# Kernel optimization log

Measured on AMD Instinct MI355X. Metric: run time of the kernel, lower is better.

Reference implementation:

```python
import jax, jax.numpy as jnp
import numpy as np

N_WIRES = 16
VAR_DEPTH = 2
BATCH = 16


def _param_sizes():
    sizes = []
    n = N_WIRES
    lay = 0
    while n > 1:
        sizes.append(4 * int(np.ceil(N_WIRES / 2 ** lay)) * VAR_DEPTH)
        n = (n + 1) // 2
        lay += 1
    return sizes  # [128, 64, 32, 16]


def _apply_1q(psi, gate, w):
    # psi: (B, 2, ..., 2); gate: (2,2) complex; wire w lives on axis w+1
    psi = jnp.moveaxis(psi, w + 1, -1)
    psi = jnp.einsum('...j,ij->...i', psi, gate)
    return jnp.moveaxis(psi, -1, w + 1)


def _rx(psi, th, w):
    c = jnp.cos(th / 2).astype(jnp.complex64)
    s = jnp.sin(th / 2).astype(jnp.complex64)
    gate = jnp.stack([jnp.stack([c, -1j * s]), jnp.stack([-1j * s, c])])
    return _apply_1q(psi, gate, w)


def _rz(psi, th, w):
    ph = jnp.exp(0.5j * th * jnp.array([-1.0, 1.0], jnp.float32)).astype(jnp.complex64)
    shape = [1] * psi.ndim
    shape[w + 1] = 2
    return psi * ph.reshape(shape)


def _rzz(psi, th, wa, wb):
    # diag(e^{-i t/2}, e^{i t/2}, e^{i t/2}, e^{-i t/2}) -> sign = -1 if bits equal else +1
    sgn = jnp.array([[-1.0, 1.0], [1.0, -1.0]], jnp.float32)
    ph = jnp.exp(0.5j * th * sgn).astype(jnp.complex64)  # symmetric, transpose-safe
    a, b = min(wa, wb) + 1, max(wa, wb) + 1
    shape = [1] * psi.ndim
    shape[a] = 2
    shape[b] = 2
    return psi * ph.reshape(shape)


def _cnot(psi, c, t):
    p0 = jax.lax.slice_in_dim(psi, 0, 1, axis=c + 1)
    p1 = jax.lax.slice_in_dim(psi, 1, 2, axis=c + 1)
    return jnp.concatenate([p0, jnp.flip(p1, axis=t + 1)], axis=c + 1)


def _conv_layer(psi, params, active):
    n = len(active)
    for d in range(VAR_DEPTH):
        for j in range(n):
            base = 4 * j + d * 4 * n
            psi = _rx(psi, params[base + 0], active[j])
            psi = _rz(psi, params[base + 1], active[j])
            psi = _rx(psi, params[base + 2], active[j])
        for bg in (0, 1):
            for j in range(bg, n, 2):
                jn = (j + 1) % n  # ring coupling (wraps last->first)
                base = 4 * j + d * 4 * n
                psi = _rzz(psi, params[base + 3], active[j], active[jn])
    return psi


def _pool(psi, active):
    for j in range(0, len(active), 2):
        if j + 1 < len(active):
            psi = _cnot(psi, active[j], active[j + 1])
    return psi, active[::2]


def _forward(psi, params_list):
    active = list(range(N_WIRES))
    for p in params_list:
        psi = _conv_layer(psi, p, active)
        if len(active) > 1:
            psi, active = _pool(psi, active)
    w = active[0]  # measure Z on the surviving wire (wire 0)
    prob = psi.real ** 2 + psi.imag ** 2
    axes = tuple(a for a in range(1, psi.ndim) if a != w + 1)
    p2 = prob.sum(axis=axes)  # (B, 2)
    return p2[:, 0] - p2[:, 1]


def setup_inputs() -> dict:
    key = jax.random.key(0)
    ks = jax.random.split(key, 8)
    dim = 2 ** N_WIRES
    x_re = jax.random.normal(ks[0], (BATCH, dim), dtype=jnp.float32)
    x_im = jax.random.normal(ks[1], (BATCH, dim), dtype=jnp.float32)
    nrm = jnp.sqrt(jnp.sum(x_re ** 2 + x_im ** 2, axis=1, keepdims=True))
    x_re = x_re / nrm
    x_im = x_im / nrm
    sizes = _param_sizes()
    two_pi = 2.0 * np.pi
    params = [jax.random.uniform(ks[2 + i], (sizes[i],), dtype=jnp.float32) * two_pi
              for i in range(len(sizes))]
    return {"x_re": x_re, "x_im": x_im,
            "params0": params[0], "params1": params[1],
            "params2": params[2], "params3": params[3]}


def reference(x_re, x_im, params0, params1, params2, params3):
    psi = (x_re + 1j * x_im).astype(jnp.complex64)
    psi = psi.reshape((BATCH,) + (2,) * N_WIRES)
    return _forward(psi, [params0, params1, params2, params3])
```

## Files before the change

kernel.cpp:

```cpp
#include <hip/hip_runtime.h>


#define DEV __device__ __forceinline__

__device__ static const unsigned char G_CP[60] = {
  15,14,13,12,11,10,9,8,7,6,5,4,3,2,1,0,
  15,14,13,12,11,10,9,8,7,6,5,4,3,2,1,0,
  15,13,11,9,7,5,3,1,
  15,13,11,9,7,5,3,1,
  15,11,7,3,
  15,11,7,3,
  15,7,
  15,7
};
__device__ static const unsigned char G_CQ[60] = {
  14,13,12,11,10,9,8,7,6,5,4,3,2,1,0,15,
  14,13,12,11,10,9,8,7,6,5,4,3,2,1,0,15,
  13,11,9,7,5,3,1,15,
  13,11,9,7,5,3,1,15,
  11,7,3,15,
  11,7,3,15,
  7,15,
  7,15
};

DEV float2 F2(float x, float y){ float2 r; r.x = x; r.y = y; return r; }
DEV float2 cmulf(float2 a, float2 b){ return F2(a.x*b.x - a.y*b.y, a.x*b.y + a.y*b.x); }
DEV int swz(int j){ return j ^ ((j>>4)&15) ^ ((j>>8)&15); }
DEV int sw2(int m){
  return m ^ ((m>>9)&1) ^ (((m>>11)&1)<<1)
           ^ ((((m>>3)&1)^((m>>8)&1))<<2)
           ^ ((((m>>4)&1)^((m>>5)&1)^((m>>10)&1))<<3);
}

#if __has_builtin(__builtin_amdgcn_permlane32_swap)
#define HAVE_PLS 1
DEV void plswap01(float &x0, float &x1){
  auto r = __builtin_amdgcn_permlane32_swap(__float_as_uint(x0), __float_as_uint(x1), false, false);
  x0 = __uint_as_float((unsigned)r[0]);
  x1 = __uint_as_float((unsigned)r[1]);
}
#else
#define HAVE_PLS 0
#endif

template<int SB>
DEV void gate4(float2* a, const float* __restrict__ g){
  float u00r=g[0],u00i=g[1],u01r=g[2],u01i=g[3],u10r=g[4],u10i=g[5],u11r=g[6],u11i=g[7];
  #pragma unroll
  for (int m=0;m<2;m++){
    int i0 = (SB==0) ? (m<<1) : m;
    int i1 = i0 | (1<<SB);
    float2 x0=a[i0], x1=a[i1];
    a[i0] = F2(u00r*x0.x - u00i*x0.y + u01r*x1.x - u01i*x1.y,
               u00r*x0.y + u00i*x0.x + u01r*x1.y + u01i*x1.x);
    a[i1] = F2(u10r*x0.x - u10i*x0.y + u11r*x1.x - u11i*x1.y,
               u10r*x0.y + u10i*x0.x + u11r*x1.y + u11i*x1.x);
  }
}

DEV void lgate(float2* a, const float* __restrict__ g, int mask, int lane){
  bool h = (lane & mask) != 0;
  float Ar = h ? g[6] : g[0], Ai = h ? g[7] : g[1];
  float Br = h ? g[4] : g[2], Bi = h ? g[5] : g[3];
  #pragma unroll
  for (int s=0;s<4;s++){
    float px = __shfl_xor(a[s].x, mask);
    float py = __shfl_xor(a[s].y, mask);
    a[s] = F2(Ar*a[s].x - Ai*a[s].y + Br*px - Bi*py,
              Ar*a[s].y + Ai*a[s].x + Br*py + Bi*px);
  }
}

DEV void lgate32(float2* a, const float* __restrict__ g, int lane){
#if HAVE_PLS
  bool h = (lane & 32) != 0;
  float c0r = h ? g[4] : g[0], c0i = h ? g[5] : g[1];
  float c1r = h ? g[6] : g[2], c1i = h ? g[7] : g[3];
  #pragma unroll
  for (int s=0;s<4;s++){
    float x0x = a[s].x, x1x = a[s].x, x0y = a[s].y, x1y = a[s].y;
    plswap01(x0x, x1x); plswap01(x0y, x1y);
    a[s] = F2(c0r*x0x - c0i*x0y + c1r*x1x - c1i*x1y,
              c0r*x0y + c0i*x0x + c1r*x1y + c1i*x1x);
  }
#else
  lgate(a, g, 32, lane);
#endif
}

DEV void cswap(float2* a, int cmask, int tmask, int lane){
  bool c = (lane & cmask) != 0;
  #pragma unroll
  for (int s=0;s<4;s++){
    float px = __shfl_xor(a[s].x, tmask);
    float py = __shfl_xor(a[s].y, tmask);
    if (c){ a[s].x = px; a[s].y = py; }
  }
}

template<int C0,int N0,int C1,int N1,unsigned M0,unsigned M1>
DEV void diagx(float2* a, const float* __restrict__ hh, unsigned Ib){
  const unsigned rm = M0|M1;
  float base = 0.f;
  #pragma unroll
  for (int k=C0;k<C0+N0;k++){
    const int p=G_CP[k], q=G_CQ[k];
    if (!(((1u<<p)|(1u<<q)) & rm)){
      float h = hh[k];
      base += (((Ib>>p)^(Ib>>q))&1u) ? h : -h;
    }
  }
  #pragma unroll
  for (int k=C1;k<C1+N1;k++){
    const int p=G_CP[k], q=G_CQ[k];
    if (!(((1u<<p)|(1u<<q)) & rm)){
      float h = hh[k];
      base += (((Ib>>p)^(Ib>>q))&1u) ? h : -h;
    }
  }
  #pragma unroll
  for (int r=0;r<4;r++){
    unsigned Ir = Ib ^ ((r&1)?M0:0u) ^ ((r&2)?M1:0u);
    float ph = base;
    #pragma unroll
    for (int k=C0;k<C0+N0;k++){
      const int p=G_CP[k], q=G_CQ[k];
      if (((1u<<p)|(1u<<q)) & rm){
        float h = hh[k];
        ph += (((Ir>>p)^(Ir>>q))&1u) ? h : -h;
      }
    }
    #pragma unroll
    for (int k=C1;k<C1+N1;k++){
      const int p=G_CP[k], q=G_CQ[k];
      if (((1u<<p)|(1u<<q)) & rm){
        float h = hh[k];
        ph += (((Ir>>p)^(Ir>>q))&1u) ? h : -h;
      }
    }
    float c, s;
    __sincosf(ph, &s, &c);
    a[r] = cmulf(a[r], F2(c, s));
  }
}

DEV void build_entry(float* sh, const float* __restrict__ p0, const float* __restrict__ p1,
                     const float* __restrict__ p2, const float* __restrict__ p3, int g){
  int d, j, n; const float* P;
  if (g < 32)      { n=16; d=(g>>4)&1; j=g&15; P=p0; }
  else if (g < 48) { n=8;  d=(g>>3)&1; j=g&7;  P=p1; }
  else if (g < 56) { n=4;  d=(g>>2)&1; j=g&3;  P=p2; }
  else             { n=2;  d=(g>>1)&1; j=g&1;  P=p3; }
  int base = 4*j + 4*n*d;
  float th0 = P[base+0], th1 = P[base+1], th2 = P[base+2], th3 = P[base+3];
  float c0,s0,ca,sa,c2,s2;
  sincosf(0.5f*th0, &s0, &c0);
  sincosf(0.5f*th1, &sa, &ca);
  sincosf(0.5f*th2, &s2, &c2);
  float B00r =  ca*c0, B00i = -sa*c0;
  float B01r = -sa*s0, B01i = -ca*s0;
  float B10r =  sa*s0, B10i = -ca*s0;
  float B11r =  ca*c0, B11i =  sa*c0;
  float* o8 = sh + g*8;
  o8[0]=c2*B00r + s2*B10i; o8[1]=c2*B00i - s2*B10r;
  o8[2]=c2*B01r + s2*B11i; o8[3]=c2*B01i - s2*B11r;
  o8[4]=s2*B00i + c2*B10r; o8[5]=-s2*B00r + c2*B10i;
  o8[6]=s2*B01i + c2*B11r; o8[7]=-s2*B01r + c2*B11i;
  sh[480 + g] = 0.5f*th3;
}

__global__ __launch_bounds__(1024, 4)
void k_pa(const float* __restrict__ xre, const float* __restrict__ xim,
          const float* __restrict__ pp0, const float* __restrict__ pp1,
          const float* __restrict__ pp2, const float* __restrict__ pp3,
          float* __restrict__ tbl, float2* __restrict__ st, float* __restrict__ out){
  const int t = threadIdx.x, lane = t & 63, wv = t >> 6;
  const int batch = blockIdx.x >> 4, o = blockIdx.x & 15;
  const unsigned hi = ((unsigned)batch<<16) | ((unsigned)o<<12);
  __shared__ float2 lds[4096];
  __shared__ float sh[544];
  float2 a[4];
  {
    unsigned base = hi | ((unsigned)t<<2);
    float4 re = *(const float4*)(xre + base);
    float4 im = *(const float4*)(xim + base);
    a[0]=F2(re.x,im.x); a[1]=F2(re.y,im.y); a[2]=F2(re.z,im.z); a[3]=F2(re.w,im.w);
  }
  if (t < 60) build_entry(sh, pp0, pp1, pp2, pp3, t);
  if (blockIdx.x == 0 && t >= 64 && t < 80) out[t - 64] = 0.f;
  __syncthreads();
  if (blockIdx.x == 0){
    for (int i = t; i < 540; i += 1024) tbl[i] = sh[i];
  }
  #define LTB(i) (sh + (i)*8)
  const float* HH = sh + 480;
  gate4<0>(a, LTB(15)); gate4<1>(a, LTB(14));
  lgate(a, LTB(13),1,lane); lgate(a, LTB(12),2,lane);
  lgate(a, LTB(11),4,lane); lgate(a, LTB(10),8,lane);
  lgate(a, LTB(9),16,lane); lgate32(a, LTB(8),lane);
  const unsigned IbA = ((unsigned)o<<12) | ((unsigned)wv<<8) | ((unsigned)lane<<2);
  diagx<8,7,0,0,1u,2u>(a, HH, IbA);
  gate4<1>(a, LTB(30));
  lgate(a, LTB(29),1,lane); lgate(a, LTB(28),2,lane);
  lgate(a, LTB(27),4,lane); lgate(a, LTB(26),8,lane);
  lgate(a, LTB(25),16,lane);
  diagx<25,5,0,0,1u,2u>(a, HH, IbA);
  cswap(a,2,1,lane);
  cswap(a,8,4,lane);
  #pragma unroll
  for (int s=0;s<4;s++) lds[swz((t<<2)|s)] = a[s];
  __syncthreads();
  const int idxR = (wv&15) | (((lane>>4)&1)<<4) | (((lane>>5)&1)<<5)
                 | (((lane>>2)&1)<<6) | (((lane>>3)&1)<<7)
                 | ((lane&1)<<8) | (((lane>>1)&1)<<9);
  #pragma unroll
  for (int s=0;s<4;s++) a[s] = lds[swz(idxR | ((s&1)<<10) | (((s>>1)&1)<<11))];
  lgate(a, LTB(7),1,lane); lgate(a, LTB(6),2,lane);
  gate4<0>(a, LTB(5)); gate4<1>(a, LTB(4));
  const unsigned IbB = ((unsigned)o<<12) | (unsigned)idxR;
  diagx<4,4,0,0,1024u,2048u>(a, HH, IbB);
  lgate(a, LTB(24),8,lane);
  lgate(a, LTB(23),1,lane); lgate(a, LTB(22),2,lane);
  gate4<0>(a, LTB(21));
  diagx<21,4,0,0,1024u,2048u>(a, HH, IbB);
  cswap(a,8,4,lane);
  cswap(a,2,1,lane);
  {
    unsigned sb = hi | ((unsigned)wv<<8) | ((unsigned)lane<<2);
    float4 v0, v1;
    v0.x=a[0].x; v0.y=a[0].y; v0.z=a[1].x; v0.w=a[1].y;
    v1.x=a[2].x; v1.y=a[2].y; v1.z=a[3].x; v1.w=a[3].y;
    *(float4*)(st + sb) = v0;
    *(float4*)(st + sb + 2) = v1;
  }
  #undef LTB
}

#define TBL(i) (tbl + (i)*8)

__global__ __launch_bounds__(1024, 4)
void k_pb(const float* __restrict__ tbl, float2* __restrict__ st, float* __restrict__ out){
  const int t = threadIdx.x, lane = t & 63, wv = t >> 6;
  const int batch = blockIdx.x >> 4, o = blockIdx.x & 15;
  __shared__ float2 lds[4096];
  __shared__ float red[16];
  const float* HH = tbl + 480;
  const unsigned opart = ((unsigned)(o&1)<<2) | ((unsigned)((o>>1)&1)<<4)
                       | ((unsigned)((o>>2)&1)<<6) | ((unsigned)((o>>3)&1)<<8);
  float2 a[4];
  {
    unsigned gb = ((unsigned)batch<<16)
      | (((unsigned)(o>>3)&1)<<2) | (((unsigned)(o>>2)&1)<<4)
      | (((unsigned)(o>>1)&1)<<6) | (((unsigned)o&1)<<10)
      | (((unsigned)(wv>>3)&1)<<3) | (((unsigned)(wv>>2)&1)<<5)
      | (((unsigned)(wv>>1)&1)<<7) | (((unsigned)wv&1)<<11)
      | (((unsigned)(lane>>4)&1)<<8) | (((unsigned)(lane>>5)&1)<<9)
      | (((unsigned)lane&1)<<12) | (((unsigned)(lane>>1)&1)<<13)
      | (((unsigned)(lane>>2)&1)<<14) | (((unsigned)(lane>>3)&1)<<15);
    const float4* sp = (const float4*)(st + gb);
    float4 lo = sp[0], hi4 = sp[1];
    a[0]=F2(lo.x,lo.y); a[1]=F2(lo.z,lo.w); a[2]=F2(hi4.x,hi4.y); a[3]=F2(hi4.z,hi4.w);
  }
  const unsigned IbA = opart
    | (((unsigned)lane&1)<<12) | (((unsigned)(lane>>1)&1)<<13)
    | (((unsigned)(lane>>2)&1)<<14) | (((unsigned)(lane>>3)&1)<<15)
    | (((unsigned)(lane>>4)&1)<<0) | (((unsigned)(lane>>5)&1)<<1)
    | (((unsigned)wv&1)<<3) | (((unsigned)(wv>>1)&1)<<5)
    | (((unsigned)(wv>>2)&1)<<7) | (((unsigned)(wv>>3)&1)<<9);
  lgate(a, TBL(3),1,lane); lgate(a, TBL(2),2,lane);
  lgate(a, TBL(1),4,lane); lgate(a, TBL(0),8,lane);
  diagx<0,4,15,1,1024u,2048u>(a, HH, IbA);
  lgate(a, TBL(31),16,lane);
  gate4<1>(a, TBL(20));
  lgate(a, TBL(19),1,lane); lgate(a, TBL(18),2,lane);
  lgate(a, TBL(17),4,lane); lgate(a, TBL(16),8,lane);
  diagx<16,5,30,2,1024u,2048u>(a, HH, IbA);
  cswap(a,8,4,lane);
  cswap(a,2,1,lane);
  { float2 tmp=a[2]; a[2]=a[3]; a[3]=tmp; }
  cswap(a,32,16,lane);
  const int idxW = ((lane>>4)&1) | (((lane>>5)&1)<<1)
                 | ((wv&1)<<2) | (((wv>>1)&1)<<3) | (((wv>>2)&1)<<4) | (((wv>>3)&1)<<5)
                 | ((lane&1)<<8) | (((lane>>1)&1)<<9)
                 | (((lane>>2)&1)<<10) | (((lane>>3)&1)<<11);
  #pragma unroll
  for (int s=0;s<4;s++) lds[sw2(idxW | ((s&1)<<6) | (((s>>1)&1)<<7))] = a[s];
  __syncthreads();
  const int idxR = (wv&1) | (((wv>>1)&1)<<6) | (((wv>>2)&1)<<8) | (((wv>>3)&1)<<10)
                 | ((lane&1)<<3) | (((lane>>1)&1)<<4) | (((lane>>2)&1)<<5)
                 | (((lane>>3)&1)<<7) | (((lane>>4)&1)<<9) | (((lane>>5)&1)<<11);
  #pragma unroll
  for (int s=0;s<4;s++) a[s] = lds[sw2(idxR | ((s&1)<<1) | (((s>>1)&1)<<2))];
  const unsigned IbB = opart
    | (((unsigned)wv&1)<<0) | (((unsigned)(wv>>1)&1)<<10)
    | (((unsigned)(wv>>2)&1)<<12) | (((unsigned)(wv>>3)&1)<<14)
    | (((unsigned)lane&1)<<5) | (((unsigned)(lane>>1)&1)<<7)
    | (((unsigned)(lane>>2)&1)<<9) | (((unsigned)(lane>>3)&1)<<11)
    | (((unsigned)(lane>>4)&1)<<13) | (((unsigned)(lane>>5)&1)<<15);
  gate4<0>(a, TBL(39)); gate4<1>(a, TBL(38));
  lgate(a, TBL(37),1,lane); lgate(a, TBL(36),2,lane); lgate(a, TBL(35),4,lane);
  lgate(a, TBL(34),8,lane); lgate(a, TBL(33),16,lane); lgate32(a, TBL(32),lane);
  diagx<32,8,0,0,2u,8u>(a, HH, IbB);
  gate4<0>(a, TBL(47)); gate4<1>(a, TBL(46));
  lgate(a, TBL(45),1,lane); lgate(a, TBL(44),2,lane); lgate(a, TBL(43),4,lane);
  lgate(a, TBL(42),8,lane); lgate(a, TBL(41),16,lane); lgate32(a, TBL(40),lane);
  diagx<40,8,0,0,2u,8u>(a, HH, IbB);
  cswap(a,32,16,lane); cswap(a,8,4,lane); cswap(a,2,1,lane);
  { float2 tmp=a[2]; a[2]=a[3]; a[3]=tmp; }
  lgate32(a, TBL(48),lane); lgate(a, TBL(49),8,lane); lgate(a, TBL(50),2,lane);
  gate4<1>(a, TBL(51));
  diagx<48,4,0,0,2u,8u>(a, HH, IbB);
  lgate32(a, TBL(52),lane); lgate(a, TBL(53),8,lane); lgate(a, TBL(54),2,lane);
  gate4<1>(a, TBL(55));
  diagx<52,4,0,0,2u,8u>(a, HH, IbB);
  cswap(a,32,8,lane);
  if (lane & 2){
    float2 t0=a[0]; a[0]=a[2]; a[2]=t0;
    float2 t1=a[1]; a[1]=a[3]; a[3]=t1;
  }
  lgate32(a, TBL(56),lane); lgate(a, TBL(57),2,lane);
  diagx<56,2,0,0,2u,8u>(a, HH, IbB);
  lgate32(a, TBL(58),lane);
  float sl = 0.f;
  #pragma unroll
  for (int s=0;s<4;s++) sl += a[s].x*a[s].x + a[s].y*a[s].y;
  float sg = (lane & 32) ? -sl : sl;
  #pragma unroll
  for (int off=32; off>0; off>>=1) sg += __shfl_down(sg, off);
  if ((t & 63) == 0) red[wv] = sg;
  __syncthreads();
  if (t == 0){
    float tot = 0.f;
    #pragma unroll
    for (int w=0; w<16; w++) tot += red[w];
    atomicAdd(out + batch, tot);
  }
}

extern "C" void kernel_launch(void* const* d_in, const int* in_sizes, int n_in,
                              void* d_out, int out_size, void* d_ws, size_t ws_size,
                              hipStream_t stream) {
  const float* xre = (const float*)d_in[0];
  const float* xim = (const float*)d_in[1];
  const float* p0  = (const float*)d_in[2];
  const float* p1  = (const float*)d_in[3];
  const float* p2  = (const float*)d_in[4];
  const float* p3  = (const float*)d_in[5];
  float* out = (float*)d_out;
  float2* st = (float2*)d_ws;
  float* tbl = (float*)((char*)d_ws + (8u<<20));

  k_pa<<<256, 1024, 0, stream>>>(xre, xim, p0, p1, p2, p3, tbl, st, out);
  k_pb<<<256, 1024, 0, stream>>>(tbl, st, out);
}
```

Baseline: 105.0 us.

## Precompute RZZ cos/sin, vectorize gate coefficient loads, stage table in LDS

Each RZZ diagonal phase now takes one sincos of the base phase per thread and applies the remaining per-element couplings as complex multiplies with precomputed cos/sin pairs. This replaces four sincos calls per diagx. The gate table rows are reordered so each lane can fetch its coefficients with a single float4 load instead of selects over scalar loads. The second kernel copies the parameter table from global memory into shared memory once per block instead of reading it from global throughout. This adds an extra sync and more shared memory use, and the chained complex multiplies may shift numerical accuracy slightly.

After: 106.2 us, median of 2. No clear change (+1.2%).

```diff
diff --git a/kernel.cpp b/kernel.cpp
--- a/kernel.cpp
+++ b/kernel.cpp
@@ -46,7 +46,10 @@
 
 template<int SB>
 DEV void gate4(float2* a, const float* __restrict__ g){
-  float u00r=g[0],u00i=g[1],u01r=g[2],u01i=g[3],u10r=g[4],u10i=g[5],u11r=g[6],u11i=g[7];
+  const float4 lo = *(const float4*)g;
+  const float4 hi = *(const float4*)(g + 4);
+  float u00r=lo.x,u00i=lo.y,u01r=lo.z,u01i=lo.w;
+  float u11r=hi.x,u11i=hi.y,u10r=hi.z,u10i=hi.w;
   #pragma unroll
   for (int m=0;m<2;m++){
     int i0 = (SB==0) ? (m<<1) : m;
@@ -60,9 +63,8 @@
 }
 
 DEV void lgate(float2* a, const float* __restrict__ g, int mask, int lane){
-  bool h = (lane & mask) != 0;
-  float Ar = h ? g[6] : g[0], Ai = h ? g[7] : g[1];
-  float Br = h ? g[4] : g[2], Bi = h ? g[5] : g[3];
+  const float4 cf = *(const float4*)(g + ((lane & mask) ? 4 : 0));
+  float Ar=cf.x, Ai=cf.y, Br=cf.z, Bi=cf.w;
   #pragma unroll
   for (int s=0;s<4;s++){
     float px = __shfl_xor(a[s].x, mask);
@@ -75,8 +77,9 @@
 DEV void lgate32(float2* a, const float* __restrict__ g, int lane){
 #if HAVE_PLS
   bool h = (lane & 32) != 0;
-  float c0r = h ? g[4] : g[0], c0i = h ? g[5] : g[1];
-  float c1r = h ? g[6] : g[2], c1i = h ? g[7] : g[3];
+  const float4 cf = *(const float4*)(g + (h ? 4 : 0));
+  float c0r = h ? cf.z : cf.x, c0i = h ? cf.w : cf.y;
+  float c1r = h ? cf.x : cf.z, c1i = h ? cf.y : cf.w;
   #pragma unroll
   for (int s=0;s<4;s++){
     float x0x = a[s].x, x1x = a[s].x, x0y = a[s].y, x1y = a[s].y;
@@ -100,15 +103,16 @@
 }
 
 template<int C0,int N0,int C1,int N1,unsigned M0,unsigned M1>
-DEV void diagx(float2* a, const float* __restrict__ hh, unsigned Ib){
+DEV void diagv(float2* a, const float* __restrict__ hh, const float* __restrict__ cs, unsigned Ib){
   const unsigned rm = M0|M1;
-  float base = 0.f;
+  float b0 = 0.f, b1 = 0.f;
   #pragma unroll
   for (int k=C0;k<C0+N0;k++){
     const int p=G_CP[k], q=G_CQ[k];
     if (!(((1u<<p)|(1u<<q)) & rm)){
       float h = hh[k];
-      base += (((Ib>>p)^(Ib>>q))&1u) ? h : -h;
+      float v = (((Ib>>p)^(Ib>>q))&1u) ? h : -h;
+      if (k & 1) b1 += v; else b0 += v;
     }
   }
   #pragma unroll
@@ -116,32 +120,37 @@
     const int p=G_CP[k], q=G_CQ[k];
     if (!(((1u<<p)|(1u<<q)) & rm)){
       float h = hh[k];
-      base += (((Ib>>p)^(Ib>>q))&1u) ? h : -h;
+      float v = (((Ib>>p)^(Ib>>q))&1u) ? h : -h;
+      if (k & 1) b1 += v; else b0 += v;
     }
   }
+  float cb, sb;
+  __sincosf(b0 + b1, &sb, &cb);
   #pragma unroll
   for (int r=0;r<4;r++){
     unsigned Ir = Ib ^ ((r&1)?M0:0u) ^ ((r&2)?M1:0u);
-    float ph = base;
+    float Fr = cb, Fi = sb;
     #pragma unroll
     for (int k=C0;k<C0+N0;k++){
       const int p=G_CP[k], q=G_CQ[k];
       if (((1u<<p)|(1u<<q)) & rm){
-        float h = hh[k];
-        ph += (((Ir>>p)^(Ir>>q))&1u) ? h : -h;
+        float ck = cs[2*k], sk = cs[2*k+1];
+        float ss = (((Ir>>p)^(Ir>>q))&1u) ? sk : -sk;
+        float nr = Fr*ck - Fi*ss, ni = Fr*ss + Fi*ck;
+        Fr = nr; Fi = ni;
       }
     }
     #pragma unroll
     for (int k=C1;k<C1+N1;k++){
       const int p=G_CP[k], q=G_CQ[k];
       if (((1u<<p)|(1u<<q)) & rm){
-        float h = hh[k];
-        ph += (((Ir>>p)^(Ir>>q))&1u) ? h : -h;
+        float ck = cs[2*k], sk = cs[2*k+1];
+        float ss = (((Ir>>p)^(Ir>>q))&1u) ? sk : -sk;
+        float nr = Fr*ck - Fi*ss, ni = Fr*ss + Fi*ck;
+        Fr = nr; Fi = ni;
       }
     }
-    float c, s;
-    __sincosf(ph, &s, &c);
-    a[r] = cmulf(a[r], F2(c, s));
+    a[r] = cmulf(a[r], F2(Fr, Fi));
   }
 }
 
@@ -165,9 +174,13 @@
   float* o8 = sh + g*8;
   o8[0]=c2*B00r + s2*B10i; o8[1]=c2*B00i - s2*B10r;
   o8[2]=c2*B01r + s2*B11i; o8[3]=c2*B01i - s2*B11r;
-  o8[4]=s2*B00i + c2*B10r; o8[5]=-s2*B00r + c2*B10i;
-  o8[6]=s2*B01i + c2*B11r; o8[7]=-s2*B01r + c2*B11i;
+  o8[4]=s2*B01i + c2*B11r; o8[5]=-s2*B01r + c2*B11i;
+  o8[6]=s2*B00i + c2*B10r; o8[7]=-s2*B00r + c2*B10i;
   sh[480 + g] = 0.5f*th3;
+  float ch, shn;
+  sincosf(0.5f*th3, &shn, &ch);
+  sh[544 + 2*g]     = ch;
+  sh[544 + 2*g + 1] = shn;
 }
 
 __global__ __launch_bounds__(1024, 4)
@@ -179,7 +192,7 @@
   const int batch = blockIdx.x >> 4, o = blockIdx.x & 15;
   const unsigned hi = ((unsigned)batch<<16) | ((unsigned)o<<12);
   __shared__ float2 lds[4096];
-  __shared__ float sh[544];
+  __shared__ float sh[672];
   float2 a[4];
   {
     unsigned base = hi | ((unsigned)t<<2);
@@ -191,21 +204,22 @@
   if (blockIdx.x == 0 && t >= 64 && t < 80) out[t - 64] = 0.f;
   __syncthreads();
   if (blockIdx.x == 0){
-    for (int i = t; i < 540; i += 1024) tbl[i] = sh[i];
+    for (int i = t; i < 664; i += 1024) tbl[i] = sh[i];
   }
   #define LTB(i) (sh + (i)*8)
   const float* HH = sh + 480;
+  const float* CS = sh + 544;
   gate4<0>(a, LTB(15)); gate4<1>(a, LTB(14));
   lgate(a, LTB(13),1,lane); lgate(a, LTB(12),2,lane);
   lgate(a, LTB(11),4,lane); lgate(a, LTB(10),8,lane);
   lgate(a, LTB(9),16,lane); lgate32(a, LTB(8),lane);
   const unsigned IbA = ((unsigned)o<<12) | ((unsigned)wv<<8) | ((unsigned)lane<<2);
-  diagx<8,7,0,0,1u,2u>(a, HH, IbA);
+  diagv<8,7,0,0,1u,2u>(a, HH, CS, IbA);
   gate4<1>(a, LTB(30));
   lgate(a, LTB(29),1,lane); lgate(a, LTB(28),2,lane);
   lgate(a, LTB(27),4,lane); lgate(a, LTB(26),8,lane);
   lgate(a, LTB(25),16,lane);
-  diagx<25,5,0,0,1u,2u>(a, HH, IbA);
+  diagv<25,5,0,0,1u,2u>(a, HH, CS, IbA);
   cswap(a,2,1,lane);
   cswap(a,8,4,lane);
   #pragma unroll
@@ -219,11 +233,11 @@
   lgate(a, LTB(7),1,lane); lgate(a, LTB(6),2,lane);
   gate4<0>(a, LTB(5)); gate4<1>(a, LTB(4));
   const unsigned IbB = ((unsigned)o<<12) | (unsigned)idxR;
-  diagx<4,4,0,0,1024u,2048u>(a, HH, IbB);
+  diagv<4,4,0,0,1024u,2048u>(a, HH, CS, IbB);
   lgate(a, LTB(24),8,lane);
   lgate(a, LTB(23),1,lane); lgate(a, LTB(22),2,lane);
   gate4<0>(a, LTB(21));
-  diagx<21,4,0,0,1024u,2048u>(a, HH, IbB);
+  diagv<21,4,0,0,1024u,2048u>(a, HH, CS, IbB);
   cswap(a,8,4,lane);
   cswap(a,2,1,lane);
   {
@@ -237,15 +251,13 @@
   #undef LTB
 }
 
-#define TBL(i) (tbl + (i)*8)
-
 __global__ __launch_bounds__(1024, 4)
 void k_pb(const float* __restrict__ tbl, float2* __restrict__ st, float* __restrict__ out){
   const int t = threadIdx.x, lane = t & 63, wv = t >> 6;
   const int batch = blockIdx.x >> 4, o = blockIdx.x & 15;
   __shared__ float2 lds[4096];
+  __shared__ float shB[672];
   __shared__ float red[16];
-  const float* HH = tbl + 480;
   const unsigned opart = ((unsigned)(o&1)<<2) | ((unsigned)((o>>1)&1)<<4)
                        | ((unsigned)((o>>2)&1)<<6) | ((unsigned)((o>>3)&1)<<8);
   float2 a[4];
@@ -260,8 +272,13 @@
       | (((unsigned)(lane>>2)&1)<<14) | (((unsigned)(lane>>3)&1)<<15);
     const float4* sp = (const float4*)(st + gb);
     float4 lo = sp[0], hi4 = sp[1];
+    if (t < 664) shB[t] = tbl[t];
     a[0]=F2(lo.x,lo.y); a[1]=F2(lo.z,lo.w); a[2]=F2(hi4.x,hi4.y); a[3]=F2(hi4.z,hi4.w);
   }
+  __syncthreads();
+  #define TBL(i) (shB + (i)*8)
+  const float* HH = shB + 480;
+  const float* CS = shB + 544;
   const unsigned IbA = opart
     | (((unsigned)lane&1)<<12) | (((unsigned)(lane>>1)&1)<<13)
     | (((unsigned)(lane>>2)&1)<<14) | (((unsigned)(lane>>3)&1)<<15)
@@ -270,16 +287,16 @@
     | (((unsigned)(wv>>2)&1)<<7) | (((unsigned)(wv>>3)&1)<<9);
   lgate(a, TBL(3),1,lane); lgate(a, TBL(2),2,lane);
   lgate(a, TBL(1),4,lane); lgate(a, TBL(0),8,lane);
-  diagx<0,4,15,1,1024u,2048u>(a, HH, IbA);
+  diagv<0,4,15,1,1024u,2048u>(a, HH, CS, IbA);
   lgate(a, TBL(31),16,lane);
   gate4<1>(a, TBL(20));
   lgate(a, TBL(19),1,lane); lgate(a, TBL(18),2,lane);
   lgate(a, TBL(17),4,lane); lgate(a, TBL(16),8,lane);
-  diagx<16,5,30,2,1024u,2048u>(a, HH, IbA);
+  diagv<16,5,30,2,1024u,2048u>(a, HH, CS, IbA);
   cswap(a,8,4,lane);
   cswap(a,2,1,lane);
+  cswap(a,32,16,lane);
   { float2 tmp=a[2]; a[2]=a[3]; a[3]=tmp; }
-  cswap(a,32,16,lane);
   const int idxW = ((lane>>4)&1) | (((lane>>5)&1)<<1)
                  | ((wv&1)<<2) | (((wv>>1)&1)<<3) | (((wv>>2)&1)<<4) | (((wv>>3)&1)<<5)
                  | ((lane&1)<<8) | (((lane>>1)&1)<<9)
@@ -301,26 +318,26 @@
   gate4<0>(a, TBL(39)); gate4<1>(a, TBL(38));
   lgate(a, TBL(37),1,lane); lgate(a, TBL(36),2,lane); lgate(a, TBL(35),4,lane);
   lgate(a, TBL(34),8,lane); lgate(a, TBL(33),16,lane); lgate32(a, TBL(32),lane);
-  diagx<32,8,0,0,2u,8u>(a, HH, IbB);
+  diagv<32,8,0,0,2u,8u>(a, HH, CS, IbB);
   gate4<0>(a, TBL(47)); gate4<1>(a, TBL(46));
   lgate(a, TBL(45),1,lane); lgate(a, TBL(44),2,lane); lgate(a, TBL(43),4,lane);
   lgate(a, TBL(42),8,lane); lgate(a, TBL(41),16,lane); lgate32(a, TBL(40),lane);
-  diagx<40,8,0,0,2u,8u>(a, HH, IbB);
+  diagv<40,8,0,0,2u,8u>(a, HH, CS, IbB);
   cswap(a,32,16,lane); cswap(a,8,4,lane); cswap(a,2,1,lane);
   { float2 tmp=a[2]; a[2]=a[3]; a[3]=tmp; }
   lgate32(a, TBL(48),lane); lgate(a, TBL(49),8,lane); lgate(a, TBL(50),2,lane);
   gate4<1>(a, TBL(51));
-  diagx<48,4,0,0,2u,8u>(a, HH, IbB);
+  diagv<48,4,0,0,2u,8u>(a, HH, CS, IbB);
   lgate32(a, TBL(52),lane); lgate(a, TBL(53),8,lane); lgate(a, TBL(54),2,lane);
   gate4<1>(a, TBL(55));
-  diagx<52,4,0,0,2u,8u>(a, HH, IbB);
+  diagv<52,4,0,0,2u,8u>(a, HH, CS, IbB);
   cswap(a,32,8,lane);
   if (lane & 2){
     float2 t0=a[0]; a[0]=a[2]; a[2]=t0;
     float2 t1=a[1]; a[1]=a[3]; a[3]=t1;
   }
   lgate32(a, TBL(56),lane); lgate(a, TBL(57),2,lane);
-  diagx<56,2,0,0,2u,8u>(a, HH, IbB);
+  diagv<56,2,0,0,2u,8u>(a, HH, CS, IbB);
   lgate32(a, TBL(58),lane);
   float sl = 0.f;
   #pragma unroll
@@ -336,6 +353,7 @@
     for (int w=0; w<16; w++) tot += red[w];
     atomicAdd(out + batch, tot);
   }
+  #undef TBL
 }
 
 extern "C" void kernel_launch(void* const* d_in, const int* in_sizes, int n_in,
```
